# Performance work log

Measured on AMD Instinct MI355X. Metric: run time of the kernel, lower is better.

The kernel has to match this reference:

```python
import jax, jax.numpy as jnp
import numpy as np

B, N, C, F, O = 32, 2048, 8, 128, 128


def setup_inputs() -> dict:
    key = jax.random.key(0)
    k1, k2, k3, k4, k5, k6 = jax.random.split(key, 6)
    nodes = jax.random.normal(k1, (B, N, F), dtype=jnp.float32)
    children = jax.random.randint(k2, (B, N, C), 0, N, dtype=jnp.int32)
    w_t = jax.random.normal(k3, (F, O), dtype=jnp.float32) * 0.05
    w_l = jax.random.normal(k4, (F, O), dtype=jnp.float32) * 0.05
    w_r = jax.random.normal(k5, (F, O), dtype=jnp.float32) * 0.05
    b = jax.random.normal(k6, (O,), dtype=jnp.float32) * 0.05
    return {"nodes": nodes, "children": children, "w_t": w_t, "w_l": w_l, "w_r": w_r, "b": b}


def reference(nodes, children, w_t, w_l, w_r, b):
    Bb, Nn, Ff = nodes.shape
    Cc = children.shape[2]
    dt = nodes.dtype

    # --- children tensor: index 0 maps to zero vector ---
    lookup = jnp.concatenate([jnp.zeros((Bb, 1, Ff), dt), nodes[:, 1:, :]], axis=1)
    batch_idx = jnp.arange(Bb)[:, None, None]
    child_vecs = lookup[batch_idx, children]                      # [B,N,C,F]
    tree = jnp.concatenate([nodes[:, :, None, :], child_vecs], axis=2)  # [B,N,C+1,F]

    # --- coefficients ---
    ch_f = children.astype(dt)
    c_t = jnp.broadcast_to(
        jnp.concatenate([jnp.ones((1, 1, 1), dt), jnp.zeros((1, 1, Cc), dt)], axis=2),
        (Bb, Nn, Cc + 1))                                          # [B,N,C+1]
    num_sib = jnp.count_nonzero(children, axis=2, keepdims=True).astype(dt)  # [B,N,1]
    mask = jnp.concatenate(
        [jnp.zeros((Bb, Nn, 1), dt), jnp.minimum(ch_f, 1.0)], axis=2)        # [B,N,C+1]
    child_indices = jnp.arange(-1.0, Cc, 1.0, dtype=dt)[None, None, :] * mask
    singles = jnp.concatenate(
        [jnp.zeros((Bb, Nn, 1), dt),
         jnp.full((Bb, Nn, 1), 0.5, dt),
         jnp.zeros((Bb, Nn, Cc - 1), dt)], axis=2)
    is_single = num_sib == 1.0
    denom = jnp.where(is_single, 1.0, num_sib - 1.0)  # safe divide, matches tf.where select
    c_r = jnp.where(is_single, singles, (1.0 - c_t) * (child_indices / denom))
    c_l = (1.0 - c_t) * (1.0 - c_r) * mask
    coef = jnp.stack([c_t, c_r, c_l], axis=3)                      # [B,N,C+1,3]

    # --- weighted aggregation + small GEMM ---
    agg = jnp.einsum('bncf,bnck->bnkf', tree, coef)                # [B,N,3,F]
    w = jnp.stack([w_t, w_r, w_l], axis=0)                         # [3,F,O]
    out = jnp.einsum('bnkf,kfo->bno', agg, w)
    return jax.nn.relu(out + b)
```

## Files before the change

kernel.cpp:

```cpp
#include <hip/hip_runtime.h>

typedef unsigned short ushort_t;
typedef __attribute__((ext_vector_type(8))) short short8;
typedef __attribute__((ext_vector_type(4))) float float4v;
typedef __attribute__((ext_vector_type(2))) unsigned int uint2v;

#define Bn 32
#define Nn 2048
#define Cn 8
#define Fn 128
#define On 128
#define Kn 384
#define MT 64
#define LDSK 392
#define NBLK ((Bn * Nn) / MT)

__device__ __forceinline__ ushort_t f2bf(float x) {
  unsigned u = __float_as_uint(x);
  u += 0x7fffu + ((u >> 16) & 1u);
  return (ushort_t)(u >> 16);
}

__device__ __forceinline__ unsigned cvt_pk_bf16(float lo, float hi) {
  unsigned r;
  asm("v_cvt_pk_bf16_f32 %0, %1, %2" : "=v"(r) : "v"(lo), "v"(hi));
  return r;
}

__device__ __forceinline__ uint2v pack4(float4v v) {
  uint2v r;
  r.x = cvt_pk_bf16(v.x, v.y);
  r.y = cvt_pk_bf16(v.z, v.w);
  return r;
}

__global__ void prep_w_kernel(const float* __restrict__ w_t,
                              const float* __restrict__ w_l,
                              const float* __restrict__ w_r,
                              ushort_t* __restrict__ wsw) {
  int t = blockIdx.x * blockDim.x + threadIdx.x;
  if (t >= 6144) return;
  int lane = t & 63;
  int r = t >> 6;
  int ks = r % 12;
  int q = r / 12;
  int col = q * 16 + (lane & 15);
  int kbase = ((lane >> 4) * 8) + ks * 32;
  ushort_t* dst = wsw + (size_t)t * 8;
#pragma unroll
  for (int j = 0; j < 8; ++j) {
    int k = kbase + j;
    const float* src = (k < Fn) ? w_t : (k < 2 * Fn) ? w_r : w_l;
    int f = k & (Fn - 1);
    dst[j] = f2bf(src[f * On + col]);
  }
}

__device__ __forceinline__ void issue_row(const float* __restrict__ nodes,
                                          int g, int ln,
                                          const int4& a, const int4& b,
                                          float4v (&dst)[9]) {
  const int base_row = g & ~(Nn - 1);
  const float4v* np = (const float4v*)nodes;
  dst[0] = np[(size_t)g * (Fn / 4) + ln];
  const int id[Cn] = {a.x, a.y, a.z, a.w, b.x, b.y, b.z, b.w};
#pragma unroll
  for (int c = 0; c < Cn; ++c) {
    const int ix = id[c] & (Nn - 1);
    dst[1 + c] = np[(size_t)(base_row + ix) * (Fn / 4) + ln];
  }
}

__device__ __forceinline__ void compute_row(ushort_t* __restrict__ agg,
                                            int row, int ln,
                                            const int4& a, const int4& b,
                                            const float4v (&v)[9]) {
  const int id[Cn] = {a.x, a.y, a.z, a.w, b.x, b.y, b.z, b.w};
  int ns = 0;
#pragma unroll
  for (int c = 0; c < Cn; ++c) ns += (id[c] != 0) ? 1 : 0;
  const bool single = (ns == 1);
  const float rden = (ns > 1) ? (1.0f / (float)(ns - 1)) : 0.0f;

  float4v rr = {0.f, 0.f, 0.f, 0.f};
  float4v ms = {0.f, 0.f, 0.f, 0.f};
#pragma unroll
  for (int c = 0; c < Cn; ++c) {
    const float m = (id[c] != 0) ? 1.0f : 0.0f;
    float cr = single ? ((c == 0) ? 0.5f : 0.0f) : ((float)c * rden);
    cr *= m;
    const float4v vc = v[1 + c];
    rr += cr * vc;
    ms += m * vc;
  }
  const float4v ll = ms - rr;

  ushort_t* arow = agg + row * LDSK + ln * 4;
  *(uint2v*)(arow)          = pack4(v[0]);
  *(uint2v*)(arow + Fn)     = pack4(rr);
  *(uint2v*)(arow + 2 * Fn) = pack4(ll);
}

__global__ __launch_bounds__(512, 4)
void tree_conv_kernel(const float* __restrict__ nodes,
                      const int* __restrict__ children,
                      const ushort_t* __restrict__ wsw,
                      const float* __restrict__ bias,
                      float* __restrict__ out) {
  __shared__ __align__(16) ushort_t agg[MT * LDSK];

  const int tid = threadIdx.x;

  const int sb = ((blockIdx.x & 7) << 7) | (blockIdx.x >> 3);

  {
    const int grp = tid >> 5;
    const int ln = tid & 31;
    const int g0 = sb * MT + grp;

    int4 ca[4], cb[4];
#define LDCH(i)                                                              \
  {                                                                          \
    const int4* chv = (const int4*)(children + (size_t)(g0 + (i)*16) * Cn);  \
    ca[i] = chv[0];                                                          \
    cb[i] = chv[1];                                                          \
  }
    LDCH(0) LDCH(1)

    float4v v0[9], v1[9];
    issue_row(nodes, g0 + 0 * 16, ln, ca[0], cb[0], v0);
    LDCH(2)
    issue_row(nodes, g0 + 1 * 16, ln, ca[1], cb[1], v1);
    LDCH(3)
    compute_row(agg, 0 * 16 + grp, ln, ca[0], cb[0], v0);
    issue_row(nodes, g0 + 2 * 16, ln, ca[2], cb[2], v0);
    compute_row(agg, 1 * 16 + grp, ln, ca[1], cb[1], v1);
    issue_row(nodes, g0 + 3 * 16, ln, ca[3], cb[3], v1);
    compute_row(agg, 2 * 16 + grp, ln, ca[2], cb[2], v0);
    compute_row(agg, 3 * 16 + grp, ln, ca[3], cb[3], v1);
#undef LDCH
  }

  const int lane = tid & 63;
  const int ct = tid >> 6;
  const int l15 = lane & 15;
  const int quad = lane >> 4;

  short8 bf[12];
  const short8* bbase = (const short8*)wsw + lane;
#pragma unroll
  for (int ks = 0; ks < 12; ++ks) bf[ks] = bbase[(ct * 12 + ks) * 64];
  const float bb = bias[ct * 16 + l15];

  asm volatile("s_waitcnt lgkmcnt(0)" ::: "memory");
  __builtin_amdgcn_s_barrier();
  asm volatile("" ::: "memory");

#pragma unroll
  for (int mt = 0; mt < 4; ++mt) {
    const ushort_t* ar = agg + (mt * 16 + l15) * LDSK + quad * 8;
    short8 af[12];
#pragma unroll
    for (int ks = 0; ks < 12; ++ks) af[ks] = *(const short8*)(ar + ks * 32);

    float4v acc = {0.f, 0.f, 0.f, 0.f};
#pragma unroll
    for (int ks = 0; ks < 12; ++ks)
      acc = __builtin_amdgcn_mfma_f32_16x16x32_bf16(af[ks], bf[ks], acc, 0, 0, 0);

    const int grow0 = sb * MT + mt * 16 + quad * 4;
#pragma unroll
    for (int r2 = 0; r2 < 4; ++r2) {
      out[(size_t)(grow0 + r2) * On + ct * 16 + l15] = fmaxf(acc[r2] + bb, 0.f);
    }
  }
}

extern "C" void kernel_launch(void* const* d_in, const int* in_sizes, int n_in,
                              void* d_out, int out_size, void* d_ws, size_t ws_size,
                              hipStream_t stream) {
  const float* nodes = (const float*)d_in[0];
  const int* children = (const int*)d_in[1];
  const float* w_t = (const float*)d_in[2];
  const float* w_l = (const float*)d_in[3];
  const float* w_r = (const float*)d_in[4];
  const float* bias = (const float*)d_in[5];
  float* out = (float*)d_out;
  ushort_t* wsw = (ushort_t*)d_ws;

  prep_w_kernel<<<24, 256, 0, stream>>>(w_t, w_l, w_r, wsw);
  tree_conv_kernel<<<NBLK, 512, 0, stream>>>(nodes, children, wsw, bias, out);
}
```

Before: 110.8 us.

## Gather rows with full wavefronts using float2 loads and deeper row pipeline

The gather phase now gives each 64-lane wavefront 8 consecutive rows and has every lane load a float2 instead of a float4 from half a wavefront. Children index loads are software-pipelined three rows ahead across a two-buffer row rotation. The launch-bounds occupancy target goes from 4 to 5, and the MFMA loop streams LDS fragments in pairs instead of loading all 12 up front, which lowers register pressure. The aim is more gathers in flight per CU and better latency hiding. The cost is smaller memory transactions per lane and possible register spills under the tighter bound.

```diff
diff --git a/kernel.cpp b/kernel.cpp
--- a/kernel.cpp
+++ b/kernel.cpp
@@ -3,7 +3,7 @@
 typedef unsigned short ushort_t;
 typedef __attribute__((ext_vector_type(8))) short short8;
 typedef __attribute__((ext_vector_type(4))) float float4v;
-typedef __attribute__((ext_vector_type(2))) unsigned int uint2v;
+typedef __attribute__((ext_vector_type(2))) float float2v;
 
 #define Bn 32
 #define Nn 2048
@@ -24,13 +24,6 @@
 __device__ __forceinline__ unsigned cvt_pk_bf16(float lo, float hi) {
   unsigned r;
   asm("v_cvt_pk_bf16_f32 %0, %1, %2" : "=v"(r) : "v"(lo), "v"(hi));
-  return r;
-}
-
-__device__ __forceinline__ uint2v pack4(float4v v) {
-  uint2v r;
-  r.x = cvt_pk_bf16(v.x, v.y);
-  r.y = cvt_pk_bf16(v.z, v.w);
   return r;
 }
 
@@ -56,25 +49,25 @@
   }
 }
 
-__device__ __forceinline__ void issue_row(const float* __restrict__ nodes,
-                                          int g, int ln,
-                                          const int4& a, const int4& b,
-                                          float4v (&dst)[9]) {
+__device__ __forceinline__ void issue_row2(const float* __restrict__ nodes,
+                                           int g, int ln,
+                                           const int4& a, const int4& b,
+                                           float2v (&dst)[9]) {
   const int base_row = g & ~(Nn - 1);
-  const float4v* np = (const float4v*)nodes;
-  dst[0] = np[(size_t)g * (Fn / 4) + ln];
+  const float2v* np = (const float2v*)nodes;
+  dst[0] = np[(size_t)g * (Fn / 2) + ln];
   const int id[Cn] = {a.x, a.y, a.z, a.w, b.x, b.y, b.z, b.w};
 #pragma unroll
   for (int c = 0; c < Cn; ++c) {
     const int ix = id[c] & (Nn - 1);
-    dst[1 + c] = np[(size_t)(base_row + ix) * (Fn / 4) + ln];
-  }
-}
-
-__device__ __forceinline__ void compute_row(ushort_t* __restrict__ agg,
-                                            int row, int ln,
-                                            const int4& a, const int4& b,
-                                            const float4v (&v)[9]) {
+    dst[1 + c] = np[(size_t)(base_row + ix) * (Fn / 2) + ln];
+  }
+}
+
+__device__ __forceinline__ void compute_row2(ushort_t* __restrict__ agg,
+                                             int row, int ln,
+                                             const int4& a, const int4& b,
+                                             const float2v (&v)[9]) {
   const int id[Cn] = {a.x, a.y, a.z, a.w, b.x, b.y, b.z, b.w};
   int ns = 0;
 #pragma unroll
@@ -82,26 +75,26 @@
   const bool single = (ns == 1);
   const float rden = (ns > 1) ? (1.0f / (float)(ns - 1)) : 0.0f;
 
-  float4v rr = {0.f, 0.f, 0.f, 0.f};
-  float4v ms = {0.f, 0.f, 0.f, 0.f};
+  float2v rr = {0.f, 0.f};
+  float2v ms = {0.f, 0.f};
 #pragma unroll
   for (int c = 0; c < Cn; ++c) {
     const float m = (id[c] != 0) ? 1.0f : 0.0f;
     float cr = single ? ((c == 0) ? 0.5f : 0.0f) : ((float)c * rden);
     cr *= m;
-    const float4v vc = v[1 + c];
+    const float2v vc = v[1 + c];
     rr += cr * vc;
     ms += m * vc;
   }
-  const float4v ll = ms - rr;
-
-  ushort_t* arow = agg + row * LDSK + ln * 4;
-  *(uint2v*)(arow)          = pack4(v[0]);
-  *(uint2v*)(arow + Fn)     = pack4(rr);
-  *(uint2v*)(arow + 2 * Fn) = pack4(ll);
-}
-
-__global__ __launch_bounds__(512, 4)
+  const float2v ll = ms - rr;
+
+  ushort_t* arow = agg + row * LDSK + ln * 2;
+  *(unsigned*)(arow)          = cvt_pk_bf16(v[0].x, v[0].y);
+  *(unsigned*)(arow + Fn)     = cvt_pk_bf16(rr.x, rr.y);
+  *(unsigned*)(arow + 2 * Fn) = cvt_pk_bf16(ll.x, ll.y);
+}
+
+__global__ __launch_bounds__(512, 5)
 void tree_conv_kernel(const float* __restrict__ nodes,
                       const int* __restrict__ children,
                       const ushort_t* __restrict__ wsw,
@@ -113,60 +106,93 @@
 
   const int sb = ((blockIdx.x & 7) << 7) | (blockIdx.x >> 3);
 
+  const int wv = tid >> 6;
+  const int ln = tid & 63;
+
   {
-    const int grp = tid >> 5;
-    const int ln = tid & 31;
-    const int g0 = sb * MT + grp;
-
-    int4 ca[4], cb[4];
-#define LDCH(i)                                                              \
+    const int g0 = sb * MT + wv * 8;
+
+    int4 pa0, pb0, pa1, pb1, pa2, pb2;
+#define LDCH(A, B, i)                                                        \
   {                                                                          \
-    const int4* chv = (const int4*)(children + (size_t)(g0 + (i)*16) * Cn);  \
-    ca[i] = chv[0];                                                          \
-    cb[i] = chv[1];                                                          \
-  }
-    LDCH(0) LDCH(1)
-
-    float4v v0[9], v1[9];
-    issue_row(nodes, g0 + 0 * 16, ln, ca[0], cb[0], v0);
-    LDCH(2)
-    issue_row(nodes, g0 + 1 * 16, ln, ca[1], cb[1], v1);
-    LDCH(3)
-    compute_row(agg, 0 * 16 + grp, ln, ca[0], cb[0], v0);
-    issue_row(nodes, g0 + 2 * 16, ln, ca[2], cb[2], v0);
-    compute_row(agg, 1 * 16 + grp, ln, ca[1], cb[1], v1);
-    issue_row(nodes, g0 + 3 * 16, ln, ca[3], cb[3], v1);
-    compute_row(agg, 2 * 16 + grp, ln, ca[2], cb[2], v0);
-    compute_row(agg, 3 * 16 + grp, ln, ca[3], cb[3], v1);
+    const int4* p4 = (const int4*)(children + (size_t)(g0 + (i)) * Cn);      \
+    A = p4[0];                                                               \
+    B = p4[1];                                                               \
+  }
+    LDCH(pa0, pb0, 0) LDCH(pa1, pb1, 1) LDCH(pa2, pb2, 2)
+
+    float2v v0[9], v1[9];
+    issue_row2(nodes, g0 + 0, ln, pa0, pb0, v0);
+    issue_row2(nodes, g0 + 1, ln, pa1, pb1, v1);
+
+    compute_row2(agg, wv * 8 + 0, ln, pa0, pb0, v0);
+    LDCH(pa0, pb0, 3)
+    issue_row2(nodes, g0 + 2, ln, pa2, pb2, v0);
+
+    compute_row2(agg, wv * 8 + 1, ln, pa1, pb1, v1);
+    LDCH(pa1, pb1, 4)
+    issue_row2(nodes, g0 + 3, ln, pa0, pb0, v1);
+
+    compute_row2(agg, wv * 8 + 2, ln, pa2, pb2, v0);
+    LDCH(pa2, pb2, 5)
+    issue_row2(nodes, g0 + 4, ln, pa1, pb1, v0);
+
+    compute_row2(agg, wv * 8 + 3, ln, pa0, pb0, v1);
+    LDCH(pa0, pb0, 6)
+    issue_row2(nodes, g0 + 5, ln, pa2, pb2, v1);
+
+    compute_row2(agg, wv * 8 + 4, ln, pa1, pb1, v0);
+    LDCH(pa1, pb1, 7)
+    issue_row2(nodes, g0 + 6, ln, pa0, pb0, v0);
+
+    compute_row2(agg, wv * 8 + 5, ln, pa2, pb2, v1);
+    issue_row2(nodes, g0 + 7, ln, pa1, pb1, v1);
+
+    compute_row2(agg, wv * 8 + 6, ln, pa0, pb0, v0);
+    compute_row2(agg, wv * 8 + 7, ln, pa1, pb1, v1);
 #undef LDCH
   }
 
-  const int lane = tid & 63;
-  const int ct = tid >> 6;
-  const int l15 = lane & 15;
-  const int quad = lane >> 4;
+  const int ct = wv;
+  const int l15 = ln & 15;
+  const int quad = ln >> 4;
 
   short8 bf[12];
-  const short8* bbase = (const short8*)wsw + lane;
+  const short8* bbase = (const short8*)wsw + ln;
 #pragma unroll
   for (int ks = 0; ks < 12; ++ks) bf[ks] = bbase[(ct * 12 + ks) * 64];
   const float bb = bias[ct * 16 + l15];
 
-  asm volatile("s_waitcnt lgkmcnt(0)" ::: "memory");
-  __builtin_amdgcn_s_barrier();
-  asm volatile("" ::: "memory");
+  __syncthreads();
 
 #pragma unroll
   for (int mt = 0; mt < 4; ++mt) {
     const ushort_t* ar = agg + (mt * 16 + l15) * LDSK + quad * 8;
-    short8 af[12];
-#pragma unroll
-    for (int ks = 0; ks < 12; ++ks) af[ks] = *(const short8*)(ar + ks * 32);
-
+    short8 a0 = *(const short8*)(ar + 0 * 32);
+    short8 a1 = *(const short8*)(ar + 1 * 32);
     float4v acc = {0.f, 0.f, 0.f, 0.f};
-#pragma unroll
-    for (int ks = 0; ks < 12; ++ks)
-      acc = __builtin_amdgcn_mfma_f32_16x16x32_bf16(af[ks], bf[ks], acc, 0, 0, 0);
+    short8 c0 = *(const short8*)(ar + 2 * 32);
+    short8 c1 = *(const short8*)(ar + 3 * 32);
+    acc = __builtin_amdgcn_mfma_f32_16x16x32_bf16(a0, bf[0], acc, 0, 0, 0);
+    acc = __builtin_amdgcn_mfma_f32_16x16x32_bf16(a1, bf[1], acc, 0, 0, 0);
+    a0 = *(const short8*)(ar + 4 * 32);
+    a1 = *(const short8*)(ar + 5 * 32);
+    acc = __builtin_amdgcn_mfma_f32_16x16x32_bf16(c0, bf[2], acc, 0, 0, 0);
+    acc = __builtin_amdgcn_mfma_f32_16x16x32_bf16(c1, bf[3], acc, 0, 0, 0);
+    c0 = *(const short8*)(ar + 6 * 32);
+    c1 = *(const short8*)(ar + 7 * 32);
+    acc = __builtin_amdgcn_mfma_f32_16x16x32_bf16(a0, bf[4], acc, 0, 0, 0);
+    acc = __builtin_amdgcn_mfma_f32_16x16x32_bf16(a1, bf[5], acc, 0, 0, 0);
+    a0 = *(const short8*)(ar + 8 * 32);
+    a1 = *(const short8*)(ar + 9 * 32);
+    acc = __builtin_amdgcn_mfma_f32_16x16x32_bf16(c0, bf[6], acc, 0, 0, 0);
+    acc = __builtin_amdgcn_mfma_f32_16x16x32_bf16(c1, bf[7], acc, 0, 0, 0);
+    c0 = *(const short8*)(ar + 10 * 32);
+    c1 = *(const short8*)(ar + 11 * 32);
+    acc = __builtin_amdgcn_mfma_f32_16x16x32_bf16(a0, bf[8], acc, 0, 0, 0);
+    acc = __builtin_amdgcn_mfma_f32_16x16x32_bf16(a1, bf[9], acc, 0, 0, 0);
+    acc = __builtin_amdgcn_mfma_f32_16x16x32_bf16(c0, bf[10], acc, 0, 0, 0);
+    acc = __builtin_amdgcn_mfma_f32_16x16x32_bf16(c1, bf[11], acc, 0, 0, 0);
 
     const int grow0 = sb * MT + mt * 16 + quad * 4;
 #pragma unroll
```

New measurement: 120.4 us. 1.09x slower.

## Halve block size and overlap gather of second half-tile with GEMM of first

Applied to the files above, without the earlier changes.

The block now has 256 threads instead of 512 and processes its 64-row tile as two 32-row halves in double-buffered LDS. While the MFMA GEMM runs on the first half, loads for the second half's gather are in flight. Each wave now computes two 16-column output tiles and keeps twice as many weight fragments in registers. This is meant to hide gather latency behind matrix work. The costs are higher register pressure, fewer threads in flight to issue gather loads, and an extra barrier.

```diff
diff --git a/kernel.cpp b/kernel.cpp
--- a/kernel.cpp
+++ b/kernel.cpp
@@ -11,9 +11,10 @@
 #define Fn 128
 #define On 128
 #define Kn 384
-#define MT 64
+#define MTB 64
+#define TT 32
 #define LDSK 392
-#define NBLK ((Bn * Nn) / MT)
+#define NBLK ((Bn * Nn) / MTB)
 
 __device__ __forceinline__ ushort_t f2bf(float x) {
   unsigned u = __float_as_uint(x);
@@ -57,22 +58,22 @@
 }
 
 __device__ __forceinline__ void issue_row(const float* __restrict__ nodes,
-                                          int g, int ln,
+                                          int g, int l32,
                                           const int4& a, const int4& b,
                                           float4v (&dst)[9]) {
   const int base_row = g & ~(Nn - 1);
   const float4v* np = (const float4v*)nodes;
-  dst[0] = np[(size_t)g * (Fn / 4) + ln];
+  dst[0] = np[(size_t)g * (Fn / 4) + l32];
   const int id[Cn] = {a.x, a.y, a.z, a.w, b.x, b.y, b.z, b.w};
 #pragma unroll
   for (int c = 0; c < Cn; ++c) {
     const int ix = id[c] & (Nn - 1);
-    dst[1 + c] = np[(size_t)(base_row + ix) * (Fn / 4) + ln];
-  }
-}
-
-__device__ __forceinline__ void compute_row(ushort_t* __restrict__ agg,
-                                            int row, int ln,
+    dst[1 + c] = np[(size_t)(base_row + ix) * (Fn / 4) + l32];
+  }
+}
+
+__device__ __forceinline__ void compute_row(ushort_t* __restrict__ aggT,
+                                            int row, int l32,
                                             const int4& a, const int4& b,
                                             const float4v (&v)[9]) {
   const int id[Cn] = {a.x, a.y, a.z, a.w, b.x, b.y, b.z, b.w};
@@ -95,85 +96,120 @@
   }
   const float4v ll = ms - rr;
 
-  ushort_t* arow = agg + row * LDSK + ln * 4;
+  ushort_t* arow = aggT + row * LDSK + l32 * 4;
   *(uint2v*)(arow)          = pack4(v[0]);
   *(uint2v*)(arow + Fn)     = pack4(rr);
   *(uint2v*)(arow + 2 * Fn) = pack4(ll);
 }
 
-__global__ __launch_bounds__(512, 4)
+__device__ __forceinline__ void gemm_mt(const ushort_t* __restrict__ aggT,
+                                        int mt, int l15, int quad,
+                                        const short8 (&bf0)[12],
+                                        const short8 (&bf1)[12],
+                                        float bb0, float bb1, int ct0, int ct1,
+                                        int growbase,
+                                        float* __restrict__ out) {
+  const ushort_t* ar = aggT + (mt * 16 + l15) * LDSK + quad * 8;
+  short8 af[12];
+#pragma unroll
+  for (int ks = 0; ks < 12; ++ks) af[ks] = *(const short8*)(ar + ks * 32);
+
+  float4v a0 = {0.f, 0.f, 0.f, 0.f};
+  float4v a1 = {0.f, 0.f, 0.f, 0.f};
+#pragma unroll
+  for (int ks = 0; ks < 12; ++ks)
+    a0 = __builtin_amdgcn_mfma_f32_16x16x32_bf16(af[ks], bf0[ks], a0, 0, 0, 0);
+#pragma unroll
+  for (int ks = 0; ks < 12; ++ks)
+    a1 = __builtin_amdgcn_mfma_f32_16x16x32_bf16(af[ks], bf1[ks], a1, 0, 0, 0);
+
+  const int grow0 = growbase + mt * 16 + quad * 4;
+#pragma unroll
+  for (int r2 = 0; r2 < 4; ++r2) {
+    const size_t ro = (size_t)(grow0 + r2) * On;
+    out[ro + ct0 * 16 + l15] = fmaxf(a0[r2] + bb0, 0.f);
+    out[ro + ct1 * 16 + l15] = fmaxf(a1[r2] + bb1, 0.f);
+  }
+}
+
+__global__ __launch_bounds__(256, 2)
 void tree_conv_kernel(const float* __restrict__ nodes,
                       const int* __restrict__ children,
                       const ushort_t* __restrict__ wsw,
                       const float* __restrict__ bias,
                       float* __restrict__ out) {
-  __shared__ __align__(16) ushort_t agg[MT * LDSK];
+  __shared__ __align__(16) ushort_t agg[2][TT * LDSK];
 
   const int tid = threadIdx.x;
 
   const int sb = ((blockIdx.x & 7) << 7) | (blockIdx.x >> 3);
+  const int gbase = sb * MTB;
+
+  const int ln = tid & 63;
+  const int wv = tid >> 6;
+  const int grp = tid >> 5;
+  const int l32 = tid & 31;
+  const int l15 = ln & 15;
+  const int quad = ln >> 4;
+  const int ct0 = wv * 2, ct1 = wv * 2 + 1;
+
+  short8 bf0[12], bf1[12];
+  const short8* bbase = (const short8*)wsw + ln;
+#pragma unroll
+  for (int ks = 0; ks < 12; ++ks) bf0[ks] = bbase[(ct0 * 12 + ks) * 64];
+#pragma unroll
+  for (int ks = 0; ks < 12; ++ks) bf1[ks] = bbase[(ct1 * 12 + ks) * 64];
+  const float bb0 = bias[ct0 * 16 + l15];
+  const float bb1 = bias[ct1 * 16 + l15];
 
   {
-    const int grp = tid >> 5;
-    const int ln = tid & 31;
-    const int g0 = sb * MT + grp;
-
+    const int g0 = gbase + grp;
     int4 ca[4], cb[4];
-#define LDCH(i)                                                              \
-  {                                                                          \
-    const int4* chv = (const int4*)(children + (size_t)(g0 + (i)*16) * Cn);  \
-    ca[i] = chv[0];                                                          \
-    cb[i] = chv[1];                                                          \
-  }
-    LDCH(0) LDCH(1)
-
+#pragma unroll
+    for (int it = 0; it < 4; ++it) {
+      const int4* p4 = (const int4*)(children + (size_t)(g0 + it * 8) * Cn);
+      ca[it] = p4[0];
+      cb[it] = p4[1];
+    }
     float4v v0[9], v1[9];
-    issue_row(nodes, g0 + 0 * 16, ln, ca[0], cb[0], v0);
-    LDCH(2)
-    issue_row(nodes, g0 + 1 * 16, ln, ca[1], cb[1], v1);
-    LDCH(3)
-    compute_row(agg, 0 * 16 + grp, ln, ca[0], cb[0], v0);
-    issue_row(nodes, g0 + 2 * 16, ln, ca[2], cb[2], v0);
-    compute_row(agg, 1 * 16 + grp, ln, ca[1], cb[1], v1);
-    issue_row(nodes, g0 + 3 * 16, ln, ca[3], cb[3], v1);
-    compute_row(agg, 2 * 16 + grp, ln, ca[2], cb[2], v0);
-    compute_row(agg, 3 * 16 + grp, ln, ca[3], cb[3], v1);
-#undef LDCH
-  }
-
-  const int lane = tid & 63;
-  const int ct = tid >> 6;
-  const int l15 = lane & 15;
-  const int quad = lane >> 4;
-
-  short8 bf[12];
-  const short8* bbase = (const short8*)wsw + lane;
-#pragma unroll
-  for (int ks = 0; ks < 12; ++ks) bf[ks] = bbase[(ct * 12 + ks) * 64];
-  const float bb = bias[ct * 16 + l15];
-
-  asm volatile("s_waitcnt lgkmcnt(0)" ::: "memory");
-  __builtin_amdgcn_s_barrier();
-  asm volatile("" ::: "memory");
-
-#pragma unroll
-  for (int mt = 0; mt < 4; ++mt) {
-    const ushort_t* ar = agg + (mt * 16 + l15) * LDSK + quad * 8;
-    short8 af[12];
-#pragma unroll
-    for (int ks = 0; ks < 12; ++ks) af[ks] = *(const short8*)(ar + ks * 32);
-
-    float4v acc = {0.f, 0.f, 0.f, 0.f};
-#pragma unroll
-    for (int ks = 0; ks < 12; ++ks)
-      acc = __builtin_amdgcn_mfma_f32_16x16x32_bf16(af[ks], bf[ks], acc, 0, 0, 0);
-
-    const int grow0 = sb * MT + mt * 16 + quad * 4;
-#pragma unroll
-    for (int r2 = 0; r2 < 4; ++r2) {
-      out[(size_t)(grow0 + r2) * On + ct * 16 + l15] = fmaxf(acc[r2] + bb, 0.f);
+    issue_row(nodes, g0 + 0 * 8, l32, ca[0], cb[0], v0);
+    issue_row(nodes, g0 + 1 * 8, l32, ca[1], cb[1], v1);
+    compute_row(agg[0], 0 * 8 + grp, l32, ca[0], cb[0], v0);
+    issue_row(nodes, g0 + 2 * 8, l32, ca[2], cb[2], v0);
+    compute_row(agg[0], 1 * 8 + grp, l32, ca[1], cb[1], v1);
+    issue_row(nodes, g0 + 3 * 8, l32, ca[3], cb[3], v1);
+    compute_row(agg[0], 2 * 8 + grp, l32, ca[2], cb[2], v0);
+    compute_row(agg[0], 3 * 8 + grp, l32, ca[3], cb[3], v1);
+  }
+
+  __syncthreads();
+
+  {
+    const int g1 = gbase + TT + grp;
+    int4 ca[4], cb[4];
+#pragma unroll
+    for (int it = 0; it < 4; ++it) {
+      const int4* p4 = (const int4*)(children + (size_t)(g1 + it * 8) * Cn);
+      ca[it] = p4[0];
+      cb[it] = p4[1];
     }
-  }
+    float4v v[9];
+    issue_row(nodes, g1 + 0 * 8, l32, ca[0], cb[0], v);
+    gemm_mt(agg[0], 0, l15, quad, bf0, bf1, bb0, bb1, ct0, ct1, gbase, out);
+    compute_row(agg[1], 0 * 8 + grp, l32, ca[0], cb[0], v);
+    issue_row(nodes, g1 + 1 * 8, l32, ca[1], cb[1], v);
+    gemm_mt(agg[0], 1, l15, quad, bf0, bf1, bb0, bb1, ct0, ct1, gbase, out);
+    compute_row(agg[1], 1 * 8 + grp, l32, ca[1], cb[1], v);
+    issue_row(nodes, g1 + 2 * 8, l32, ca[2], cb[2], v);
+    compute_row(agg[1], 2 * 8 + grp, l32, ca[2], cb[2], v);
+    issue_row(nodes, g1 + 3 * 8, l32, ca[3], cb[3], v);
+    compute_row(agg[1], 3 * 8 + grp, l32, ca[3], cb[3], v);
+  }
+
+  __syncthreads();
+
+  gemm_mt(agg[1], 0, l15, quad, bf0, bf1, bb0, bb1, ct0, ct1, gbase + TT, out);
+  gemm_mt(agg[1], 1, l15, quad, bf0, bf1, bb0, bb1, ct0, ct1, gbase + TT, out);
 }
 
 extern "C" void kernel_launch(void* const* d_in, const int* in_sizes, int n_in,
@@ -189,5 +225,5 @@
   ushort_t* wsw = (ushort_t*)d_ws;
 
   prep_w_kernel<<<24, 256, 0, stream>>>(w_t, w_l, w_r, wsw);
-  tree_conv_kernel<<<NBLK, 512, 0, stream>>>(nodes, children, wsw, bias, out);
-}
+  tree_conv_kernel<<<NBLK, 256, 0, stream>>>(nodes, children, wsw, bias, out);
+}
```

New measurement: 113.1 us. 2.0% more time.
